# Performance work log

Measured on AMD Instinct MI355X. Metric: run time of the kernel, lower is better.

Reference implementation:

```python
import jax, jax.numpy as jnp
import numpy as np

E = 640000
D = 128  # out_channels
NEG_SLOPE = 0.2


def setup_inputs() -> dict:
    key = jax.random.key(0)
    k1, k2, k3 = jax.random.split(key, 3)
    Wx_i = jax.random.normal(k1, (E, D), dtype=jnp.float32)
    Wx_j = jax.random.normal(k2, (E, D), dtype=jnp.float32)
    # attention vector over concat([Wx_i, Wx_j]) -> shape [2*D]
    a = jax.random.normal(k3, (2 * D,), dtype=jnp.float32) * (1.0 / np.sqrt(2 * D))
    return {"Wx_i": Wx_i, "Wx_j": Wx_j, "a": a}


def reference(Wx_i, Wx_j, a):
    # e = LeakyReLU(a^T [Wx_i || Wx_j]) per edge, without materializing the concat
    a_src, a_dst = a[:D], a[D:]
    logits = Wx_i @ a_src + Wx_j @ a_dst  # [E]
    return jax.nn.leaky_relu(logits, negative_slope=NEG_SLOPE)
```

## Files before the change

kernel.cpp:

```cpp
#include <hip/hip_runtime.h>

#define D_DIM 128
#define NEG_SLOPE 0.2f

__global__ __launch_bounds__(256) void gat_score_kernel(
    const float* __restrict__ Wx_i,
    const float* __restrict__ Wx_j,
    const float* __restrict__ a,
    float* __restrict__ out,
    int E)
{
    const int tid = threadIdx.x;
    const int lane32 = tid & 31;
    const int rowInBlock = tid >> 5;
    const int row = blockIdx.x * 8 + rowInBlock;

    const float4 as = ((const float4*)a)[lane32];
    const float4 ad = ((const float4*)(a + D_DIM))[lane32];

    if (row < E) {
        const float4 xi = ((const float4*)(Wx_i + (size_t)row * D_DIM))[lane32];
        const float4 xj = ((const float4*)(Wx_j + (size_t)row * D_DIM))[lane32];

        float s = xi.x * as.x + xi.y * as.y + xi.z * as.z + xi.w * as.w
                + xj.x * ad.x + xj.y * ad.y + xj.z * ad.z + xj.w * ad.w;

        #pragma unroll
        for (int off = 16; off > 0; off >>= 1)
            s += __shfl_down(s, off, 32);

        if (lane32 == 0)
            out[row] = (s > 0.0f) ? s : NEG_SLOPE * s;
    }
}

extern "C" void kernel_launch(void* const* d_in, const int* in_sizes, int n_in,
                              void* d_out, int out_size, void* d_ws, size_t ws_size,
                              hipStream_t stream) {
    const float* Wx_i = (const float*)d_in[0];
    const float* Wx_j = (const float*)d_in[1];
    const float* a    = (const float*)d_in[2];
    float* out = (float*)d_out;

    const int E = out_size;
    const int rowsPerBlock = 8;
    const int grid = (E + rowsPerBlock - 1) / rowsPerBlock;

    gat_score_kernel<<<grid, 256, 0, stream>>>(Wx_i, Wx_j, a, out, E);
}
```

Measured before the change: 592.1 us.

## Process four rows per 32-lane group with grid-stride loop and fixed grid

Each 32-lane group now handles four consecutive rows per iteration, issuing eight independent float4 loads, interleaving four shuffle reductions, and writing the four results as one float4 store. The launch uses a fixed grid of 2048 blocks with a grid-stride loop in place of one block per eight rows. The aim is more memory-level parallelism per thread and less block launch and scheduling overhead on a bandwidth-bound kernel. It assumes E is a multiple of four; otherwise the loads and the float4 store run past the ends of the arrays.

```diff
diff --git a/kernel.cpp b/kernel.cpp
--- a/kernel.cpp
+++ b/kernel.cpp
@@ -10,27 +10,46 @@
     float* __restrict__ out,
     int E)
 {
-    const int tid = threadIdx.x;
-    const int lane32 = tid & 31;
-    const int rowInBlock = tid >> 5;
-    const int row = blockIdx.x * 8 + rowInBlock;
+    const int tid  = threadIdx.x;
+    const int lane = tid & 31;
+    const int group = (blockIdx.x << 3) | (tid >> 5);
+    const int numGroups = gridDim.x << 3;
 
-    const float4 as = ((const float4*)a)[lane32];
-    const float4 ad = ((const float4*)(a + D_DIM))[lane32];
+    const float4 as = ((const float4*)a)[lane];
+    const float4 ad = ((const float4*)(a + D_DIM))[lane];
 
-    if (row < E) {
-        const float4 xi = ((const float4*)(Wx_i + (size_t)row * D_DIM))[lane32];
-        const float4 xj = ((const float4*)(Wx_j + (size_t)row * D_DIM))[lane32];
+    for (int row0 = group * 4; row0 < E; row0 += numGroups * 4) {
+        const float4* pi = (const float4*)(Wx_i + (size_t)row0 * D_DIM) + lane;
+        const float4* pj = (const float4*)(Wx_j + (size_t)row0 * D_DIM) + lane;
 
-        float s = xi.x * as.x + xi.y * as.y + xi.z * as.z + xi.w * as.w
-                + xj.x * ad.x + xj.y * ad.y + xj.z * ad.z + xj.w * ad.w;
+        const float4 xi0 = pi[0],  xi1 = pi[32], xi2 = pi[64], xi3 = pi[96];
+        const float4 xj0 = pj[0],  xj1 = pj[32], xj2 = pj[64], xj3 = pj[96];
+
+        float s0 = xi0.x*as.x + xi0.y*as.y + xi0.z*as.z + xi0.w*as.w
+                 + xj0.x*ad.x + xj0.y*ad.y + xj0.z*ad.z + xj0.w*ad.w;
+        float s1 = xi1.x*as.x + xi1.y*as.y + xi1.z*as.z + xi1.w*as.w
+                 + xj1.x*ad.x + xj1.y*ad.y + xj1.z*ad.z + xj1.w*ad.w;
+        float s2 = xi2.x*as.x + xi2.y*as.y + xi2.z*as.z + xi2.w*as.w
+                 + xj2.x*ad.x + xj2.y*ad.y + xj2.z*ad.z + xj2.w*ad.w;
+        float s3 = xi3.x*as.x + xi3.y*as.y + xi3.z*as.z + xi3.w*as.w
+                 + xj3.x*ad.x + xj3.y*ad.y + xj3.z*ad.z + xj3.w*ad.w;
 
         #pragma unroll
-        for (int off = 16; off > 0; off >>= 1)
-            s += __shfl_down(s, off, 32);
+        for (int off = 16; off > 0; off >>= 1) {
+            s0 += __shfl_down(s0, off, 32);
+            s1 += __shfl_down(s1, off, 32);
+            s2 += __shfl_down(s2, off, 32);
+            s3 += __shfl_down(s3, off, 32);
+        }
 
-        if (lane32 == 0)
-            out[row] = (s > 0.0f) ? s : NEG_SLOPE * s;
+        if (lane == 0) {
+            float4 r;
+            r.x = (s0 > 0.0f) ? s0 : NEG_SLOPE * s0;
+            r.y = (s1 > 0.0f) ? s1 : NEG_SLOPE * s1;
+            r.z = (s2 > 0.0f) ? s2 : NEG_SLOPE * s2;
+            r.w = (s3 > 0.0f) ? s3 : NEG_SLOPE * s3;
+            ((float4*)out)[row0 >> 2] = r;
+        }
     }
 }
 
@@ -43,8 +62,7 @@
     float* out = (float*)d_out;
 
     const int E = out_size;
-    const int rowsPerBlock = 8;
-    const int grid = (E + rowsPerBlock - 1) / rowsPerBlock;
+    const int grid = 2048;
 
     gat_score_kernel<<<grid, 256, 0, stream>>>(Wx_i, Wx_j, a, out, E);
 }
```

After: 604.7 us. 1.02x slower.
